# Performance work log

Hardware: AMD Instinct MI355X
Metric: run time of the kernel (lower is better)

## Reference

```python
import jax, jax.numpy as jnp
import numpy as np

NUM_GROUPS = 32
NUM_HEADS = 8  # channels=512 / num_head_channels=64
EPS = 1e-5


def group_norm(x, gamma, beta):
    # x: [B, C, T]
    b, c, t = x.shape
    xg = x.reshape(b, NUM_GROUPS, (c // NUM_GROUPS) * t)
    mean = xg.mean(axis=-1, keepdims=True)
    var = xg.var(axis=-1, keepdims=True)
    xg = (xg - mean) * jax.lax.rsqrt(var + EPS)
    return xg.reshape(b, c, t) * gamma[None, :, None] + beta[None, :, None]


def setup_inputs() -> dict:
    key = jax.random.key(0)
    ks = jax.random.split(key, 8)
    B, C, H, W = 16, 512, 32, 32
    E = 1024
    x = jax.random.normal(ks[0], (B, C, H, W), dtype=jnp.float32)
    emb = jax.random.normal(ks[1], (B, E), dtype=jnp.float32)
    gn_gamma = jnp.ones((C,), jnp.float32)
    gn_beta = jnp.zeros((C,), jnp.float32)
    # FiLM: Linear(emb_channels, 2*channels), weight init std=0.001, bias zero
    emb_w = jax.random.normal(ks[2], (2 * C, E), dtype=jnp.float32) * 0.001
    emb_b = jnp.zeros((2 * C,), jnp.float32)
    # conv1x1 qkv: [3C, C]
    qkv_w = jax.random.normal(ks[3], (3 * C, C), dtype=jnp.float32) * (1.0 / np.sqrt(C))
    qkv_b = jnp.zeros((3 * C,), jnp.float32)
    # proj_out conv1x1 (zero-init in original; use small random so grads flow)
    proj_w = jax.random.normal(ks[4], (C, C), dtype=jnp.float32) * 0.02
    proj_b = jnp.zeros((C,), jnp.float32)
    return dict(x=x, emb=emb, gn_gamma=gn_gamma, gn_beta=gn_beta,
                emb_w=emb_w, emb_b=emb_b, qkv_w=qkv_w, qkv_b=qkv_b,
                proj_w=proj_w, proj_b=proj_b)


def reference(x, emb, gn_gamma, gn_beta, emb_w, emb_b, qkv_w, qkv_b, proj_w, proj_b):
    b, c, h_sp, w_sp = x.shape
    t = h_sp * w_sp
    xr = x.reshape(b, c, t)
    h = group_norm(xr, gn_gamma, gn_beta)
    # FiLM conditioning
    e = jax.nn.silu(emb) @ emb_w.T + emb_b  # [B, 2C]
    scale, shift = jnp.split(e, 2, axis=1)
    h = h * (1.0 + scale[:, :, None]) + shift[:, :, None]
    # conv1x1 QKV
    qkv = jnp.einsum('oc,bct->bot', qkv_w, h) + qkv_b[None, :, None]  # [B, 3C, T]
    ch = c // NUM_HEADS
    qkv = qkv.reshape(b * NUM_HEADS, 3 * ch, t)  # legacy head ordering
    q, k, v = jnp.split(qkv, 3, axis=1)
    s = 1.0 / jnp.sqrt(jnp.sqrt(jnp.float32(ch)))
    w = jnp.einsum('bct,bcs->bts', q * s, k * s)  # [B*H, T, T]
    w = jax.nn.softmax(w, axis=-1)
    a = jnp.einsum('bts,bcs->bct', w, v).reshape(b, c, t)
    out = jnp.einsum('oc,bct->bot', proj_w, a) + proj_b[None, :, None]
    return (xr + out).reshape(b, c, h_sp, w_sp)
```

## Files before the change

kernel.cpp:

```cpp
#include <hip/hip_runtime.h>
#include <hip/hip_bf16.h>

typedef __hip_bfloat16 bf16;
typedef __attribute__((ext_vector_type(8))) short short8;
typedef __attribute__((ext_vector_type(4))) float f32x4;
typedef __attribute__((ext_vector_type(4))) unsigned short us4;
typedef __attribute__((ext_vector_type(2))) unsigned short us2;

#define B_  16
#define C_  512
#define T_  1024
#define G_  32
#define CPG 16
#define E_  1024
#define NH  8
#define CH  64
#define CT  (C_ * T_)

__device__ __forceinline__ float b2f(bf16 v) { return __bfloat162float(v); }
__device__ __forceinline__ unsigned short fbits_fast(float v) {
  unsigned int u = __builtin_bit_cast(unsigned int, v);
  u += 0x7fff + ((u >> 16) & 1);
  return (unsigned short)(u >> 16);
}
__device__ __forceinline__ bf16 f2b_fast(float v) {
  unsigned short s = fbits_fast(v);
  return *reinterpret_cast<bf16*>(&s);
}
__device__ __forceinline__ unsigned int cvtpk(float lo, float hi) {
  unsigned int r;
  asm("v_cvt_pk_bf16_f32 %0, %1, %2" : "=v"(r) : "v"(lo), "v"(hi));
  return r;
}

__device__ __forceinline__ void gload16(const void* g, void* l) {
  __builtin_amdgcn_global_load_lds(
      (const __attribute__((address_space(1))) void*)g,
      (__attribute__((address_space(3))) void*)l, 16, 0, 0);
}

__global__ __launch_bounds__(1024) void prep_kernel(
    const float* __restrict__ qkv_w, const float* __restrict__ proj_w,
    bf16* __restrict__ wq, bf16* __restrict__ wp,
    const float* __restrict__ emb, const float* __restrict__ emb_w,
    const float* __restrict__ emb_b, float* __restrict__ e_out,
    const float* __restrict__ x, float* __restrict__ mean_buf,
    float* __restrict__ rstd_buf, int nconv) {
  __shared__ float S[B_ * E_];
  __shared__ float ss[16], ssq[16];
  int bid = blockIdx.x;
  int tid = threadIdx.x;
  if (bid < nconv) {
    int i4 = bid * 1024 + tid;
    const int NQ4 = (3 * C_ * C_) / 4;
    const float* src;
    unsigned short* dst;
    int off;
    if (i4 < NQ4) {
      src = qkv_w; dst = (unsigned short*)wq; off = i4;
    } else {
      src = proj_w; dst = (unsigned short*)wp; off = i4 - NQ4;
    }
    float4 v = *(const float4*)(src + (size_t)off * 4);
    uint2 pk = {cvtpk(v.x, v.y), cvtpk(v.z, v.w)};
    *(uint2*)(dst + (size_t)off * 4) = pk;
    return;
  }
  bid -= nconv;
  int wave = tid >> 6, lane = tid & 63;
  if (bid < 64) {
    float4* S4 = (float4*)S;
    const float4* e4 = (const float4*)emb;
    for (int i = tid; i < (B_ * E_) / 4; i += 1024) {
      float4 v = e4[i];
      float4 o;
      o.x = v.x / (1.f + __expf(-v.x));
      o.y = v.y / (1.f + __expf(-v.y));
      o.z = v.z / (1.f + __expf(-v.z));
      o.w = v.w / (1.f + __expf(-v.w));
      S4[i] = o;
    }
    __syncthreads();
    int j = bid * 16 + wave;
    const float4* w4p = (const float4*)(emb_w + (size_t)j * E_);
    float4 w4[4];
#pragma unroll
    for (int k = 0; k < 4; k++) w4[k] = w4p[k * 64 + lane];
    float bias = emb_b[j];
    for (int b = 0; b < B_; b++) {
      const float4* Sb = (const float4*)(S + b * E_);
      float acc = 0.f;
#pragma unroll
      for (int k = 0; k < 4; k++) {
        float4 s = Sb[k * 64 + lane];
        acc += w4[k].x * s.x + w4[k].y * s.y + w4[k].z * s.z + w4[k].w * s.w;
      }
#pragma unroll
      for (int off = 1; off < 64; off <<= 1) acc += __shfl_xor(acc, off, 64);
      if (lane == 0) e_out[b * (2 * C_) + j] = acc + bias;
    }
    return;
  }
  bid -= 64;
  {
    int bg = bid;
    const float4* b4 = (const float4*)(x + (size_t)bg * (CPG * T_));
    float s = 0.f, sq = 0.f;
#pragma unroll
    for (int p = 0; p < 4; p++) {
      float4 v = b4[p * 1024 + tid];
      s += v.x + v.y + v.z + v.w;
      sq += v.x * v.x + v.y * v.y + v.z * v.z + v.w * v.w;
    }
    for (int off = 32; off > 0; off >>= 1) {
      s += __shfl_down(s, off, 64);
      sq += __shfl_down(sq, off, 64);
    }
    if (lane == 0) { ss[wave] = s; ssq[wave] = sq; }
    __syncthreads();
    if (tid == 0) {
      float Sm = 0.f, Q = 0.f;
#pragma unroll
      for (int w = 0; w < 16; w++) { Sm += ss[w]; Q += ssq[w]; }
      const float inv_n = 1.f / (CPG * T_);
      float m = Sm * inv_n;
      float var = Q * inv_n - m * m;
      mean_buf[bg] = m;
      rstd_buf[bg] = rsqrtf(fmaxf(var, 0.f) + 1e-5f);
    }
  }
}

__global__ __launch_bounds__(256) void convert_one(
    const float* __restrict__ src, bf16* __restrict__ dst) {
  int i4 = blockIdx.x * 256 + threadIdx.x;
  float4 v = *(const float4*)(src + (size_t)i4 * 4);
  uint2 pk = {cvtpk(v.x, v.y), cvtpk(v.z, v.w)};
  *(uint2*)((unsigned short*)dst + (size_t)i4 * 4) = pk;
}

__global__ __launch_bounds__(256) void norm_film_t2(
    const float* __restrict__ x, const float* __restrict__ mean_buf,
    const float* __restrict__ rstd_buf, const float* __restrict__ gamma,
    const float* __restrict__ beta, const float* __restrict__ e_buf,
    bf16* __restrict__ h, int b0) {
  __shared__ unsigned short S[64][66];
  __shared__ float pm[64], pr[64], pa[64];
  int t0 = blockIdx.x * 64;
  int c0 = blockIdx.y * 64;
  int bl = blockIdx.z;
  int b = b0 + bl;
  int tid = threadIdx.x;
  if (tid < 64) {
    int c = c0 + tid;
    int g = c >> 4;
    float m = mean_buf[b * G_ + g];
    float r = rstd_buf[b * G_ + g];
    float sc = 1.f + e_buf[b * 2 * C_ + c];
    float sh = e_buf[b * 2 * C_ + C_ + c];
    pm[tid] = m;
    pr[tid] = r * gamma[c] * sc;
    pa[tid] = beta[c] * sc + sh;
  }
  __syncthreads();
  const float* xb = x + ((size_t)b * C_ + c0) * T_ + t0;
#pragma unroll
  for (int p = 0; p < 4; p++) {
    int i = p * 256 + tid;
    int cl = i >> 4, t4 = (i & 15) * 4;
    float4 v = *(const float4*)(xb + (size_t)cl * T_ + t4);
    float m = pm[cl], r = pr[cl], ad = pa[cl];
    *(unsigned int*)&S[cl][t4] = cvtpk((v.x - m) * r + ad, (v.y - m) * r + ad);
    *(unsigned int*)&S[cl][t4 + 2] =
        cvtpk((v.z - m) * r + ad, (v.w - m) * r + ad);
  }
  __syncthreads();
  unsigned short* hg = (unsigned short*)h + ((size_t)bl * T_ + t0) * C_ + c0;
#pragma unroll
  for (int p = 0; p < 2; p++) {
    int i = p * 256 + tid;
    int tr = i >> 3, c8 = (i & 7) * 8;
    unsigned int w0 = (unsigned int)S[c8 + 0][tr] |
                      ((unsigned int)S[c8 + 1][tr] << 16);
    unsigned int w1 = (unsigned int)S[c8 + 2][tr] |
                      ((unsigned int)S[c8 + 3][tr] << 16);
    unsigned int w2 = (unsigned int)S[c8 + 4][tr] |
                      ((unsigned int)S[c8 + 5][tr] << 16);
    unsigned int w3 = (unsigned int)S[c8 + 6][tr] |
                      ((unsigned int)S[c8 + 7][tr] << 16);
    int4 pk = {(int)w0, (int)w1, (int)w2, (int)w3};
    *(int4*)(hg + (size_t)tr * C_ + c8) = pk;
  }
}

#define ST_STRIDE 264
__global__ __launch_bounds__(256) void qkv_gemm_mfma5(
    const bf16* __restrict__ h, const bf16* __restrict__ wq,
    const float* __restrict__ qkv_b, bf16* __restrict__ qb,
    bf16* __restrict__ kb, bf16* __restrict__ vb, int ngroups) {
  __shared__ __align__(16) unsigned short LB[40960];
  int bid = blockIdx.x;
  int g, o;
  if ((ngroups & 7) == 0) {
    int xcd = bid & 7, j = bid >> 3;
    o = j % 24;
    int slot = j / 24;
    g = slot * 8 + xcd;
  } else {
    o = bid % 24;
    g = bid / 24;
  }
  int tst = g & 3;
  int bl = g >> 2;
  int o0 = o * 64;
  int tb = tst * 256;
  int tid = threadIdx.x;
  int wave = tid >> 6, lane = tid & 63;
  int col = lane & 15, quad = lane >> 4;
  int cs = col & 7;
  int w64 = wave * 64;
  const unsigned short* hg = (const unsigned short*)h + (size_t)bl * T_ * C_;
  const unsigned short* wg = (const unsigned short*)wq;
  char* lds = (char*)LB;
  f32x4 acc[4][4];
  for (int i = 0; i < 4; i++)
    for (int j2 = 0; j2 < 4; j2++) acc[i][j2] = f32x4{0, 0, 0, 0};

#define QSTAGE(buf, c0_)                                                      \
  do {                                                                        \
    _Pragma("unroll") for (int p = 0; p < 8; p++) {                           \
      int i_ = p * 256 + tid;                                                 \
      int row_ = i_ >> 3;                                                     \
      int sci_ = (i_ & 7) ^ (row_ & 7);                                       \
      gload16(hg + (size_t)(tb + row_) * C_ + (c0_) + sci_ * 8,               \
              lds + (buf) * 40960 + (p * 256 + wave * 64) * 16);              \
    }                                                                         \
    _Pragma("unroll") for (int p = 0; p < 2; p++) {                           \
      int i_ = p * 256 + tid;                                                 \
      int row_ = i_ >> 3;                                                     \
      int sci_ = (i_ & 7) ^ (row_ & 7);                                       \
      gload16(wg + (size_t)(o0 + row_) * C_ + (c0_) + sci_ * 8,               \
              lds + (buf) * 40960 + 32768 + (p * 256 + wave * 64) * 16);      \
    }                                                                         \
  } while (0)

  QSTAGE(0, 0);
  __syncthreads();
  int cur = 0;
  for (int kst = 0; kst < 8; kst++) {
    if (kst < 7) QSTAGE(cur ^ 1, (kst + 1) * 64);
    const unsigned short* hb = LB + cur * 20480;
    const unsigned short* wb2 = hb + 16384;
    __builtin_amdgcn_s_setprio(1);
#pragma unroll
    for (int ks = 0; ks < 2; ks++) {
      short8 af[4], bfr[4];
#pragma unroll
      for (int mt = 0; mt < 4; mt++)
        af[mt] = *(const short8*)&hb[(w64 + mt * 16 + col) * 64 +
                                     (((ks * 4 + quad) ^ cs) << 3)];
#pragma unroll
      for (int nt = 0; nt < 4; nt++)
        bfr[nt] = *(const short8*)&wb2[(nt * 16 + col) * 64 +
                                       (((ks * 4 + quad) ^ cs) << 3)];
#pragma unroll
      for (int mt = 0; mt < 4; mt++)
#pragma unroll
        for (int nt = 0; nt < 4; nt++)
          acc[mt][nt] = __builtin_amdgcn_mfma_f32_16x16x32_bf16(
              af[mt], bfr[nt], acc[mt][nt], 0, 0, 0);
    }
    __builtin_amdgcn_s_setprio(0);
    __syncthreads();
    cur ^= 1;
  }
#undef QSTAGE
  int sec = (o0 >> 6) % 3;
  int hd = o0 / 192;
  const float s = 0.35355339059327373f;
  const float sq = s * 1.4426950408889634f;
  if (sec < 2) {
    bf16* dst = (sec == 0) ? qb : kb;
    float sc = (sec == 0) ? sq : s;
    size_t hb2 = (size_t)(bl * NH + hd) * T_ * CH;
    for (int mt = 0; mt < 4; mt++) {
      for (int r = 0; r < 4; r++) {
        int t = tb + w64 + mt * 16 + quad * 4 + r;
        for (int nt = 0; nt < 4; nt++) {
          int ch = nt * 16 + col;
          dst[hb2 + (size_t)t * CH + ch] =
              f2b_fast((acc[mt][nt][r] + qkv_b[o0 + ch]) * sc);
        }
      }
    }
  } else {
    for (int mt = 0; mt < 4; mt++) {
      for (int r = 0; r < 4; r++) {
        int tl = w64 + mt * 16 + quad * 4 + r;
        for (int nt = 0; nt < 4; nt++) {
          int ch = nt * 16 + col;
          LB[ch * ST_STRIDE + tl] =
              fbits_fast(acc[mt][nt][r] + qkv_b[o0 + ch]);
        }
      }
    }
    __syncthreads();
    int rr = tid >> 2, csx = (tid & 3) * 64;
    size_t base = ((size_t)(bl * NH + hd) * CH + rr) * T_ + tb + csx;
    unsigned short* vg = (unsigned short*)vb;
    for (int j2 = 0; j2 < 8; j2++)
      *(int4*)(vg + base + j2 * 8) =
          *(const int4*)&LB[rr * ST_STRIDE + csx + j2 * 8];
  }
}

__global__ __launch_bounds__(256, 4) void attn_mfma10(
    const bf16* __restrict__ qb, const bf16* __restrict__ kb,
    const bf16* __restrict__ vb, bf16* __restrict__ a, int nbh) {
  __shared__ __align__(16) unsigned short LB[20480];
  int bid = blockIdx.x;
  int bh = bid % nbh;
  int qt0 = (bid / nbh) * 128;
  int tid = threadIdx.x;
  int wave = tid >> 6, lane = tid & 63;
  int col = lane & 15, quad = lane >> 4;
  int cs = col & 7;
  int ps = (col >> 1) & 3;
  const unsigned short* qg = (const unsigned short*)qb;
  const unsigned short* kg = (const unsigned short*)kb;
  const unsigned short* vg = (const unsigned short*)vb;
  const size_t tmaj = (size_t)bh * T_ * CH;
  const size_t cmaj = (size_t)bh * CH * T_;
  char* lds = (char*)LB;

  int qrow = qt0 + wave * 16 + col;
  short8 bq0[2], bq1[2];
#pragma unroll
  for (int u = 0; u < 2; u++) {
    const unsigned short* qp = qg + tmaj + (size_t)(qrow + u * 64) * CH;
    bq0[u] = *(const short8*)(qp + quad * 8);
    bq1[u] = *(const short8*)(qp + 32 + quad * 8);
  }
  f32x4 Ot0[4], Ot1[4];
#pragma unroll
  for (int mt = 0; mt < 4; mt++) {
    Ot0[mt] = f32x4{0, 0, 0, 0};
    Ot1[mt] = f32x4{0, 0, 0, 0};
  }
  const short ob = (short)0x3F80;
  short8 ones = {ob, ob, ob, ob, ob, ob, ob, ob};
  f32x4 La0 = f32x4{0, 0, 0, 0}, La1 = f32x4{0, 0, 0, 0};
  const f32x4 z4 = {0.f, 0.f, 0.f, 0.f};
  unsigned short* pw0 = LB + 16384 + wave * 512 + col * 32;
  unsigned short* pw1 = pw0 + 2048;

#define STAGE(buf, tt)                                                        \
  do {                                                                        \
    int s0_ = (tt) * 64;                                                      \
    const unsigned short* kt_ = kg + tmaj + (size_t)s0_ * CH;                 \
    const unsigned short* vt_ = vg + cmaj + s0_;                              \
    _Pragma("unroll") for (int cc = 0; cc < 2; cc++) {                        \
      int i_ = cc * 256 + tid;                                                \
      int row_ = i_ >> 3;                                                     \
      int sci_ = (i_ & 7) ^ (row_ & 7);                                       \
      int wb_ = (cc * 256 + wave * 64) * 16;       \
      gload16(kt_ + (size_t)row_ * CH + sci_ * 8, lds + (buf) * 8192 + wb_);  \
      gload16(vt_ + (size_t)row_ * T_ + sci_ * 8,                             \
              lds + 16384 + (buf) * 8192 + wb_);                              \
    }                                                                         \
  } while (0)

  STAGE(0, 0);
  __syncthreads();
  int cur = 0;
  for (int t = 0; t < 16; t++) {
    if (t < 15) STAGE(cur ^ 1, t + 1);
    const char* ksb = lds + cur * 8192;
    const char* vtb = lds + 16384 + cur * 8192;
    f32x4 St0[4], St1[4];
    __builtin_amdgcn_s_setprio(1);
#pragma unroll
    for (int mt = 0; mt < 4; mt++) {
      int rb = (mt * 16 + col) * 128;
      short8 ak0 = *(const short8*)(ksb + rb + ((quad ^ cs) << 4));
      short8 ak1 = *(const short8*)(ksb + rb + (((quad + 4) ^ cs) << 4));
      St0[mt] = __builtin_amdgcn_mfma_f32_16x16x32_bf16(ak0, bq0[0], z4, 0, 0, 0);
      St1[mt] = __builtin_amdgcn_mfma_f32_16x16x32_bf16(ak0, bq0[1], z4, 0, 0, 0);
      St0[mt] = __builtin_amdgcn_mfma_f32_16x16x32_bf16(ak1, bq1[0], St0[mt], 0, 0, 0);
      St1[mt] = __builtin_amdgcn_mfma_f32_16x16x32_bf16(ak1, bq1[1], St1[mt], 0, 0, 0);
    }
    __builtin_amdgcn_s_setprio(0);
#pragma unroll
    for (int mt = 0; mt < 4; mt++)
#pragma unroll
      for (int r = 0; r < 4; r++) {
        St0[mt][r] = __builtin_amdgcn_exp2f(St0[mt][r]);
        St1[mt][r] = __builtin_amdgcn_exp2f(St1[mt][r]);
      }
#pragma unroll
    for (int kc = 0; kc < 2; kc++) {
#pragma unroll
      for (int mh = 0; mh < 2; mh++) {
        int mt = kc * 2 + mh;
        int wsw = (((2 * mh + (quad >> 1)) ^ ps) << 3) + (quad & 1) * 4;
        uint2 k0 = {cvtpk(St0[mt][0], St0[mt][1]),
                    cvtpk(St0[mt][2], St0[mt][3])};
        uint2 k1 = {cvtpk(St1[mt][0], St1[mt][1]),
                    cvtpk(St1[mt][2], St1[mt][3])};
        *(uint2*)(pw0 + wsw) = k0;
        *(uint2*)(pw1 + wsw) = k1;
      }
      int rsw = (quad ^ ps) << 3;
      short8 bp0 = *(const short8*)(pw0 + rsw);
      short8 bp1 = *(const short8*)(pw1 + rsw);
      __builtin_amdgcn_s_setprio(1);
      La0 = __builtin_amdgcn_mfma_f32_16x16x32_bf16(ones, bp0, La0, 0, 0, 0);
      La1 = __builtin_amdgcn_mfma_f32_16x16x32_bf16(ones, bp1, La1, 0, 0, 0);
#pragma unroll
      for (int mt = 0; mt < 4; mt++) {
        short8 av = *(const short8*)(vtb + (mt * 16 + col) * 128 +
                                     (((kc * 4 + quad) ^ cs) << 4));
        Ot0[mt] = __builtin_amdgcn_mfma_f32_16x16x32_bf16(av, bp0, Ot0[mt], 0, 0, 0);
        Ot1[mt] = __builtin_amdgcn_mfma_f32_16x16x32_bf16(av, bp1, Ot1[mt], 0, 0, 0);
      }
      __builtin_amdgcn_s_setprio(0);
    }
    __syncthreads();
    cur ^= 1;
  }
#undef STAGE
  int bl = bh >> 3, hd = bh & 7;
  unsigned short* ag = (unsigned short*)a;
#pragma unroll
  for (int u = 0; u < 2; u++) {
    float inv = 1.f / ((u == 0) ? La0[0] : La1[0]);
    const f32x4* Ou = (u == 0) ? Ot0 : Ot1;
    size_t rowb = ((size_t)bl * T_ + qrow + u * 64) * C_ + hd * CH;
#pragma unroll
    for (int mt = 0; mt < 4; mt++) {
      uint2 pk = {cvtpk(Ou[mt][0] * inv, Ou[mt][1] * inv),
                  cvtpk(Ou[mt][2] * inv, Ou[mt][3] * inv)};
      *(uint2*)(ag + rowb + mt * 16 + quad * 4) = pk;
    }
  }
}

__global__ __launch_bounds__(256) void proj_mfma4(
    const bf16* __restrict__ a, const bf16* __restrict__ wp,
    const float* __restrict__ proj_b, const float* __restrict__ x,
    float* __restrict__ out, int b0) {
  __shared__ __align__(16) unsigned short LB[16384];
  int bl = blockIdx.z;
  int b = b0 + bl;
  int o0 = blockIdx.y * 64;
  int t0 = blockIdx.x * 64;
  int tid = threadIdx.x;
  int wave = tid >> 6, lane = tid & 63;
  int col = lane & 15, quad = lane >> 4;
  int cs = col & 7;
  int m0 = wave * 16;
  const unsigned short* ag = (const unsigned short*)a + (size_t)bl * T_ * C_;
  const unsigned short* wg = (const unsigned short*)wp;
  char* lds = (char*)LB;
  f32x4 acc[4] = {f32x4{0,0,0,0}, f32x4{0,0,0,0}, f32x4{0,0,0,0}, f32x4{0,0,0,0}};

#define PSTAGE(buf, c0_)                                                      \
  do {                                                                        \
    _Pragma("unroll") for (int cc = 0; cc < 2; cc++) {                        \
      int i_ = cc * 256 + tid;                                                \
      int row_ = i_ >> 3;                                                     \
      int sci_ = (i_ & 7) ^ (row_ & 7);                                       \
      int wb_ = (cc * 256 + wave * 64) * 16;                                  \
      gload16(ag + (size_t)(t0 + row_) * C_ + (c0_) + sci_ * 8,               \
              lds + (buf) * 16384 + wb_);                                     \
      gload16(wg + (size_t)(o0 + row_) * C_ + (c0_) + sci_ * 8,               \
              lds + (buf) * 16384 + 8192 + wb_);                              \
    }                                                                         \
  } while (0)

  PSTAGE(0, 0);
  __syncthreads();
  int cur = 0;
  for (int kst = 0; kst < 8; kst++) {
    if (kst < 7) PSTAGE(cur ^ 1, (kst + 1) * 64);
    const unsigned short* ab = LB + cur * 8192;
    const unsigned short* wb2 = ab + 4096;
    __builtin_amdgcn_s_setprio(1);
#pragma unroll
    for (int ks = 0; ks < 2; ks++) {
      short8 aw = *(const short8*)&wb2[(m0 + col) * 64 +
                                       (((ks * 4 + quad) ^ cs) << 3)];
#pragma unroll
      for (int nt = 0; nt < 4; nt++) {
        short8 ba = *(const short8*)&ab[(nt * 16 + col) * 64 +
                                        (((ks * 4 + quad) ^ cs) << 3)];
        acc[nt] = __builtin_amdgcn_mfma_f32_16x16x32_bf16(aw, ba, acc[nt], 0, 0, 0);
      }
    }
    __builtin_amdgcn_s_setprio(0);
    __syncthreads();
    cur ^= 1;
  }
#undef PSTAGE
  for (int r = 0; r < 4; r++) {
    int o = o0 + m0 + quad * 4 + r;
    float bias = proj_b[o];
    size_t rowb = ((size_t)b * C_ + o) * T_ + t0;
    for (int nt = 0; nt < 4; nt++) {
      int t = nt * 16 + col;
      out[rowb + t] = x[rowb + t] + acc[nt][r] + bias;
    }
  }
}

extern "C" void kernel_launch(void* const* d_in, const int* in_sizes, int n_in,
                              void* d_out, int out_size, void* d_ws,
                              size_t ws_size, hipStream_t stream) {
  const float* x      = (const float*)d_in[0];
  const float* emb    = (const float*)d_in[1];
  const float* gamma  = (const float*)d_in[2];
  const float* beta   = (const float*)d_in[3];
  const float* emb_w  = (const float*)d_in[4];
  const float* emb_b  = (const float*)d_in[5];
  const float* qkv_w  = (const float*)d_in[6];
  const float* qkv_b  = (const float*)d_in[7];
  const float* proj_w = (const float*)d_in[8];
  const float* proj_b = (const float*)d_in[9];
  float* out = (float*)d_out;

  const size_t BUF16 = (size_t)16 * CT * sizeof(bf16);
  const size_t FULL4 = 4 * BUF16;
  const size_t SCR   = 131072 + (size_t)4 * C_ * C_ * sizeof(bf16);

  if (ws_size >= FULL4) {
    bf16* h_buf = (bf16*)d_ws;
    bf16* q_buf = h_buf + BUF16 / sizeof(bf16);
    bf16* k_buf = q_buf + BUF16 / sizeof(bf16);
    bf16* v_buf = k_buf + BUF16 / sizeof(bf16);
    bool inWs = ws_size >= FULL4 + SCR;
    char* scr = inWs ? ((char*)d_ws + FULL4) : (char*)d_out;
    float* e_buf    = (float*)scr;
    float* mean_buf = e_buf + B_ * 2 * C_;
    float* rstd_buf = mean_buf + B_ * G_;
    bf16*  wq_bf    = (bf16*)(scr + 131072);
    bf16*  wp_bf;
    int nconv;
    if (inWs) {
      wp_bf = wq_bf + (size_t)3 * C_ * C_;
      nconv = 256;
    } else {
      wp_bf = q_buf;
      nconv = 192;
    }
    prep_kernel<<<dim3(nconv + 64 + 512), 1024, 0, stream>>>(
        qkv_w, proj_w, wq_bf, wp_bf, emb, emb_w, emb_b, e_buf, x, mean_buf,
        rstd_buf, nconv);
    norm_film_t2<<<dim3(16, 8, 16), 256, 0, stream>>>(
        x, mean_buf, rstd_buf, gamma, beta, e_buf, h_buf, 0);
    qkv_gemm_mfma5<<<dim3(24 * 64), 256, 0, stream>>>(h_buf, wq_bf, qkv_b,
                                                      q_buf, k_buf, v_buf, 64);
    attn_mfma10<<<dim3(8 * 128), 256, 0, stream>>>(q_buf, k_buf, v_buf, h_buf,
                                                   128);
    if (!inWs)
      convert_one<<<dim3(256), 256, 0, stream>>>(proj_w, wp_bf);
    proj_mfma4<<<dim3(16, 8, 16), 256, 0, stream>>>(h_buf, wp_bf, proj_b, x,
                                                    out, 0);
  } else {
    float* e_buf    = (float*)d_ws;
    float* mean_buf = e_buf + B_ * 2 * C_;
    float* rstd_buf = mean_buf + B_ * G_;
    bf16*  wq_bf    = (bf16*)((char*)d_ws + 131072);
    bf16*  wp_bf    = wq_bf + (size_t)3 * C_ * C_;
    bf16* pool = (bf16*)((char*)d_ws + SCR);
    size_t avail = ws_size > SCR ? ws_size - SCR : 0;
    int NB = 16;
    while (NB > 1 && (size_t)4 * NB * CT * sizeof(bf16) > avail) NB >>= 1;
    bf16* h_buf = pool;
    bf16* q_buf = h_buf + (size_t)NB * CT;
    bf16* k_buf = q_buf + (size_t)NB * CT;
    bf16* v_buf = k_buf + (size_t)NB * CT;

    prep_kernel<<<dim3(256 + 64 + 512), 1024, 0, stream>>>(
        qkv_w, proj_w, wq_bf, wp_bf, emb, emb_w, emb_b, e_buf, x, mean_buf,
        rstd_buf, 256);
    for (int b0 = 0; b0 < B_; b0 += NB) {
      norm_film_t2<<<dim3(16, 8, NB), 256, 0, stream>>>(
          x, mean_buf, rstd_buf, gamma, beta, e_buf, h_buf, b0);
      qkv_gemm_mfma5<<<dim3(24 * 4 * NB), 256, 0, stream>>>(
          h_buf, wq_bf, qkv_b, q_buf, k_buf, v_buf, 4 * NB);
      int nbh = NB * NH;
      attn_mfma10<<<dim3(8 * nbh), 256, 0, stream>>>(q_buf, k_buf, v_buf,
                                                     h_buf, nbh);
      proj_mfma4<<<dim3(16, 8, NB), 256, 0, stream>>>(h_buf, wp_bf, proj_b, x,
                                                      out, b0);
    }
  }
}
```

Before: 206.4 us.

## Rewrite attention inner loop with 32x32x16 MFMA and permlane P exchange

The attention kernel moves from 16x16x32 MFMA tiles to 32x32x16 tiles, with each wave owning 32 query rows. The probability matrix now goes from S accumulator layout to the PV operand layout through v_permlane32_swap in registers, so the LDS round trip for P is gone and LDS shrinks. The row-sum is kept as a per-lane scalar and reduced across half-waves at the end, replacing the extra ones-vector MFMA. The aim is fewer LDS accesses and fewer MFMA issues per tile. The cost is a larger 16-float accumulator per tile, which raises register pressure, plus a layout mapping that must be exactly right.

```diff
diff --git a/kernel.cpp b/kernel.cpp
--- a/kernel.cpp
+++ b/kernel.cpp
@@ -4,6 +4,8 @@
 typedef __hip_bfloat16 bf16;
 typedef __attribute__((ext_vector_type(8))) short short8;
 typedef __attribute__((ext_vector_type(4))) float f32x4;
+typedef __attribute__((ext_vector_type(16))) float f32x16;
+typedef __attribute__((ext_vector_type(4))) unsigned int uint4v;
 typedef __attribute__((ext_vector_type(4))) unsigned short us4;
 typedef __attribute__((ext_vector_type(2))) unsigned short us2;
 
@@ -314,18 +316,17 @@
   }
 }
 
-__global__ __launch_bounds__(256, 4) void attn_mfma10(
+__global__ __launch_bounds__(256, 4) void attn_mfma11(
     const bf16* __restrict__ qb, const bf16* __restrict__ kb,
     const bf16* __restrict__ vb, bf16* __restrict__ a, int nbh) {
-  __shared__ __align__(16) unsigned short LB[20480];
+  __shared__ __align__(16) unsigned short LB[16384];
   int bid = blockIdx.x;
   int bh = bid % nbh;
   int qt0 = (bid / nbh) * 128;
   int tid = threadIdx.x;
   int wave = tid >> 6, lane = tid & 63;
-  int col = lane & 15, quad = lane >> 4;
+  int col = lane & 31, h = lane >> 5;
   int cs = col & 7;
-  int ps = (col >> 1) & 3;
   const unsigned short* qg = (const unsigned short*)qb;
   const unsigned short* kg = (const unsigned short*)kb;
   const unsigned short* vg = (const unsigned short*)vb;
@@ -333,26 +334,16 @@
   const size_t cmaj = (size_t)bh * CH * T_;
   char* lds = (char*)LB;
 
-  int qrow = qt0 + wave * 16 + col;
-  short8 bq0[2], bq1[2];
-#pragma unroll
-  for (int u = 0; u < 2; u++) {
-    const unsigned short* qp = qg + tmaj + (size_t)(qrow + u * 64) * CH;
-    bq0[u] = *(const short8*)(qp + quad * 8);
-    bq1[u] = *(const short8*)(qp + 32 + quad * 8);
-  }
-  f32x4 Ot0[4], Ot1[4];
-#pragma unroll
-  for (int mt = 0; mt < 4; mt++) {
-    Ot0[mt] = f32x4{0, 0, 0, 0};
-    Ot1[mt] = f32x4{0, 0, 0, 0};
-  }
-  const short ob = (short)0x3F80;
-  short8 ones = {ob, ob, ob, ob, ob, ob, ob, ob};
-  f32x4 La0 = f32x4{0, 0, 0, 0}, La1 = f32x4{0, 0, 0, 0};
-  const f32x4 z4 = {0.f, 0.f, 0.f, 0.f};
-  unsigned short* pw0 = LB + 16384 + wave * 512 + col * 32;
-  unsigned short* pw1 = pw0 + 2048;
+  int qrow = qt0 + wave * 32 + col;
+  short8 bq[4];
+#pragma unroll
+  for (int kst = 0; kst < 4; kst++)
+    bq[kst] =
+        *(const short8*)(qg + tmaj + (size_t)qrow * CH + kst * 16 + h * 8);
+  f32x16 Ot0, Ot1, z16;
+#pragma unroll
+  for (int r = 0; r < 16; r++) { Ot0[r] = 0.f; Ot1[r] = 0.f; z16[r] = 0.f; }
+  float l_r = 0.f;
 
 #define STAGE(buf, tt)                                                        \
   do {                                                                        \
@@ -377,70 +368,67 @@
     if (t < 15) STAGE(cur ^ 1, t + 1);
     const char* ksb = lds + cur * 8192;
     const char* vtb = lds + 16384 + cur * 8192;
-    f32x4 St0[4], St1[4];
-    __builtin_amdgcn_s_setprio(1);
-#pragma unroll
-    for (int mt = 0; mt < 4; mt++) {
-      int rb = (mt * 16 + col) * 128;
-      short8 ak0 = *(const short8*)(ksb + rb + ((quad ^ cs) << 4));
-      short8 ak1 = *(const short8*)(ksb + rb + (((quad + 4) ^ cs) << 4));
-      St0[mt] = __builtin_amdgcn_mfma_f32_16x16x32_bf16(ak0, bq0[0], z4, 0, 0, 0);
-      St1[mt] = __builtin_amdgcn_mfma_f32_16x16x32_bf16(ak0, bq0[1], z4, 0, 0, 0);
-      St0[mt] = __builtin_amdgcn_mfma_f32_16x16x32_bf16(ak1, bq1[0], St0[mt], 0, 0, 0);
-      St1[mt] = __builtin_amdgcn_mfma_f32_16x16x32_bf16(ak1, bq1[1], St1[mt], 0, 0, 0);
-    }
-    __builtin_amdgcn_s_setprio(0);
-#pragma unroll
-    for (int mt = 0; mt < 4; mt++)
-#pragma unroll
-      for (int r = 0; r < 4; r++) {
-        St0[mt][r] = __builtin_amdgcn_exp2f(St0[mt][r]);
-        St1[mt][r] = __builtin_amdgcn_exp2f(St1[mt][r]);
-      }
-#pragma unroll
-    for (int kc = 0; kc < 2; kc++) {
-#pragma unroll
-      for (int mh = 0; mh < 2; mh++) {
-        int mt = kc * 2 + mh;
-        int wsw = (((2 * mh + (quad >> 1)) ^ ps) << 3) + (quad & 1) * 4;
-        uint2 k0 = {cvtpk(St0[mt][0], St0[mt][1]),
-                    cvtpk(St0[mt][2], St0[mt][3])};
-        uint2 k1 = {cvtpk(St1[mt][0], St1[mt][1]),
-                    cvtpk(St1[mt][2], St1[mt][3])};
-        *(uint2*)(pw0 + wsw) = k0;
-        *(uint2*)(pw1 + wsw) = k1;
-      }
-      int rsw = (quad ^ ps) << 3;
-      short8 bp0 = *(const short8*)(pw0 + rsw);
-      short8 bp1 = *(const short8*)(pw1 + rsw);
+#pragma unroll
+    for (int n = 0; n < 2; n++) {
+      f32x16 St;
+      const char* krow = ksb + (n * 32 + col) * 128;
       __builtin_amdgcn_s_setprio(1);
-      La0 = __builtin_amdgcn_mfma_f32_16x16x32_bf16(ones, bp0, La0, 0, 0, 0);
-      La1 = __builtin_amdgcn_mfma_f32_16x16x32_bf16(ones, bp1, La1, 0, 0, 0);
-#pragma unroll
-      for (int mt = 0; mt < 4; mt++) {
-        short8 av = *(const short8*)(vtb + (mt * 16 + col) * 128 +
-                                     (((kc * 4 + quad) ^ cs) << 4));
-        Ot0[mt] = __builtin_amdgcn_mfma_f32_16x16x32_bf16(av, bp0, Ot0[mt], 0, 0, 0);
-        Ot1[mt] = __builtin_amdgcn_mfma_f32_16x16x32_bf16(av, bp1, Ot1[mt], 0, 0, 0);
+      {
+        short8 ak0 = *(const short8*)(krow + ((0 + h) ^ cs) * 16);
+        St = __builtin_amdgcn_mfma_f32_32x32x16_bf16(ak0, bq[0], z16, 0, 0, 0);
+        short8 ak1 = *(const short8*)(krow + ((2 + h) ^ cs) * 16);
+        St = __builtin_amdgcn_mfma_f32_32x32x16_bf16(ak1, bq[1], St, 0, 0, 0);
+        short8 ak2 = *(const short8*)(krow + ((4 + h) ^ cs) * 16);
+        St = __builtin_amdgcn_mfma_f32_32x32x16_bf16(ak2, bq[2], St, 0, 0, 0);
+        short8 ak3 = *(const short8*)(krow + ((6 + h) ^ cs) * 16);
+        St = __builtin_amdgcn_mfma_f32_32x32x16_bf16(ak3, bq[3], St, 0, 0, 0);
       }
       __builtin_amdgcn_s_setprio(0);
+#pragma unroll
+      for (int r = 0; r < 16; r++) {
+        St[r] = __builtin_amdgcn_exp2f(St[r]);
+        l_r += St[r];
+      }
+      unsigned int w[8];
+#pragma unroll
+      for (int m = 0; m < 8; m++) w[m] = cvtpk(St[2 * m], St[2 * m + 1]);
+#pragma unroll
+      for (int tt = 0; tt < 2; tt++) {
+        unsigned int a0 = w[4 * tt + 0], b0 = w[4 * tt + 2];
+        unsigned int a1 = w[4 * tt + 1], b1 = w[4 * tt + 3];
+        asm volatile("v_permlane32_swap_b32 %0, %1" : "+v"(a0), "+v"(b0));
+        asm volatile("v_permlane32_swap_b32 %0, %1" : "+v"(a1), "+v"(b1));
+        uint4v ub = {a0, a1, b0, b1};
+        short8 bp = __builtin_bit_cast(short8, ub);
+        int sstep = n * 2 + tt;
+        int vchunk = ((2 * sstep + h) ^ cs) * 16;
+        __builtin_amdgcn_s_setprio(1);
+        short8 av0 = *(const short8*)(vtb + col * 128 + vchunk);
+        Ot0 = __builtin_amdgcn_mfma_f32_32x32x16_bf16(av0, bp, Ot0, 0, 0, 0);
+        short8 av1 = *(const short8*)(vtb + (32 + col) * 128 + vchunk);
+        Ot1 = __builtin_amdgcn_mfma_f32_32x32x16_bf16(av1, bp, Ot1, 0, 0, 0);
+        __builtin_amdgcn_s_setprio(0);
+      }
     }
     __syncthreads();
     cur ^= 1;
   }
 #undef STAGE
+  l_r += __shfl_xor(l_r, 32, 64);
+  float inv = 1.f / l_r;
   int bl = bh >> 3, hd = bh & 7;
   unsigned short* ag = (unsigned short*)a;
-#pragma unroll
-  for (int u = 0; u < 2; u++) {
-    float inv = 1.f / ((u == 0) ? La0[0] : La1[0]);
-    const f32x4* Ou = (u == 0) ? Ot0 : Ot1;
-    size_t rowb = ((size_t)bl * T_ + qrow + u * 64) * C_ + hd * CH;
-#pragma unroll
-    for (int mt = 0; mt < 4; mt++) {
-      uint2 pk = {cvtpk(Ou[mt][0] * inv, Ou[mt][1] * inv),
-                  cvtpk(Ou[mt][2] * inv, Ou[mt][3] * inv)};
-      *(uint2*)(ag + rowb + mt * 16 + quad * 4) = pk;
+  size_t rowb = ((size_t)bl * T_ + qrow) * C_ + hd * CH;
+#pragma unroll
+  for (int mch = 0; mch < 2; mch++) {
+#pragma unroll
+    for (int g = 0; g < 4; g++) {
+      float o0 = (mch ? Ot1[4 * g + 0] : Ot0[4 * g + 0]) * inv;
+      float o1 = (mch ? Ot1[4 * g + 1] : Ot0[4 * g + 1]) * inv;
+      float o2 = (mch ? Ot1[4 * g + 2] : Ot0[4 * g + 2]) * inv;
+      float o3 = (mch ? Ot1[4 * g + 3] : Ot0[4 * g + 3]) * inv;
+      uint2 pk = {cvtpk(o0, o1), cvtpk(o2, o3)};
+      *(uint2*)(ag + rowb + mch * 32 + 8 * g + 4 * h) = pk;
     }
   }
 }
@@ -559,7 +547,7 @@
         x, mean_buf, rstd_buf, gamma, beta, e_buf, h_buf, 0);
     qkv_gemm_mfma5<<<dim3(24 * 64), 256, 0, stream>>>(h_buf, wq_bf, qkv_b,
                                                       q_buf, k_buf, v_buf, 64);
-    attn_mfma10<<<dim3(8 * 128), 256, 0, stream>>>(q_buf, k_buf, v_buf, h_buf,
+    attn_mfma11<<<dim3(8 * 128), 256, 0, stream>>>(q_buf, k_buf, v_buf, h_buf,
                                                    128);
     if (!inWs)
       convert_one<<<dim3(256), 256, 0, stream>>>(proj_w, wp_bf);
@@ -589,7 +577,7 @@
       qkv_gemm_mfma5<<<dim3(24 * 4 * NB), 256, 0, stream>>>(
           h_buf, wq_bf, qkv_b, q_buf, k_buf, v_buf, 4 * NB);
       int nbh = NB * NH;
-      attn_mfma10<<<dim3(8 * nbh), 256, 0, stream>>>(q_buf, k_buf, v_buf,
+      attn_mfma11<<<dim3(8 * nbh), 256, 0, stream>>>(q_buf, k_buf, v_buf,
                                                      h_buf, nbh);
       proj_mfma4<<<dim3(16, 8, NB), 256, 0, stream>>>(h_buf, wp_bf, proj_b, x,
                                                       out, b0);
```

After: 212.7 us. 1.03x slower.
